# Kernel tuning notes

Hardware: AMD Instinct MI355X
Metric: run time of the kernel (lower is better)

The kernel has to match this reference:

```python
import jax, jax.numpy as jnp
import numpy as np

ALPHA = 0.2          # LeakyReLU negative slope
THRESHOLD = 0.5      # adjacency threshold
NEG_INF = -9e15      # same fill value as torch source


def setup_inputs() -> dict:
    key = jax.random.key(0)
    k_in, k_adj, k_W, k_a = jax.random.split(key, 4)
    B, N, C = 32, 1024, 64
    inp = jax.random.normal(k_in, (B, N, C), dtype=jnp.float32)
    adj = jax.random.uniform(k_adj, (N, N), dtype=jnp.float32)
    # xavier_uniform with gain=1.414 (as in torch init)
    gain = 1.414
    lim_W = gain * np.sqrt(6.0 / (C + C))
    W = jax.random.uniform(k_W, (C, C), dtype=jnp.float32, minval=-lim_W, maxval=lim_W)
    lim_a = gain * np.sqrt(6.0 / (2 * C + 1))
    a = jax.random.uniform(k_a, (2 * C, 1), dtype=jnp.float32, minval=-lim_a, maxval=lim_a)
    return {"input": inp, "adj": adj, "W": W, "a": a}


def reference(input, adj, W, a):
    # h: [B, N, C]
    h = jnp.matmul(input, W)
    C = W.shape[0]
    a_src = a[:C, 0]   # applied to h_i (row / query node)
    a_dst = a[C:, 0]   # applied to h_j (col / neighbor node)
    # Algebraic decomposition of a^T [h_i || h_j]: outer-sum of two [B,N] vectors.
    s_src = jnp.matmul(h, a_src)  # [B, N]
    s_dst = jnp.matmul(h, a_dst)  # [B, N]
    e = jax.nn.leaky_relu(s_src[:, :, None] + s_dst[:, None, :], negative_slope=ALPHA)  # [B,N,N]
    mask = adj > THRESHOLD  # [N, N], broadcast over batch
    attention = jax.nn.softmax(jnp.where(mask[None, :, :], e, NEG_INF), axis=2)
    h_prime = jnp.matmul(attention, h)  # [B, N, C]
    return jax.nn.elu(h_prime)
```

## Files before the change

kernel.cpp:

```cpp
#include <hip/hip_runtime.h>
#include <math.h>

#define ALPHA 0.2f
#define LOG2E 1.4426950408889634f

constexpr int B = 32, N = 1024, C = 64;

typedef __attribute__((ext_vector_type(8))) short short8;
typedef __attribute__((ext_vector_type(4))) float floatx4;

static __device__ __forceinline__ unsigned f32bf(float f) {
    unsigned u = __float_as_uint(f);
    return (u + 0x7FFFu + ((u >> 16) & 1u)) >> 16;
}

static __device__ __forceinline__ void async_copy16(void* lds_base, const void* g) {
    __builtin_amdgcn_global_load_lds(
        (const __attribute__((address_space(1))) unsigned int*)g,
        (__attribute__((address_space(3))) unsigned int*)lds_base, 16, 0, 0);
}

__global__ __launch_bounds__(256) void gat_pre(
    const float* __restrict__ input, const float* __restrict__ adj,
    const float* __restrict__ Wm, const float* __restrict__ a,
    unsigned short* __restrict__ hT, float* __restrict__ ssrc,
    float* __restrict__ sdst, unsigned long long* __restrict__ mask64)
{
    const int tid = threadIdx.x, lane = tid & 63, wave = tid >> 6;

    if (blockIdx.x >= 1024) {
        const int mb = blockIdx.x - 1024;
#pragma unroll
        for (int t = 0; t < 4; ++t) {
            const int id = mb * 16 + wave * 4 + t;
            const int i = id >> 4, jc = id & 15;
            const float av = adj[(size_t)i * N + jc * 64 + lane];
            const unsigned long long bal = __ballot(av > 0.5f);
            if (lane == 0) mask64[i * 16 + jc] = bal;
        }
        return;
    }

    __shared__ __align__(16) float W_l[64 * 65];
    __shared__ __align__(16) float a_l[128];
    __shared__ float wa_l[128];

    const int row0 = blockIdx.x * 32;
    const int b = row0 >> 10;
    const int jloc0 = row0 & 1023;
    const int m = lane & 15, kq = lane >> 4;

#pragma unroll
    for (int t = 0; t < 4; ++t) {
        const int t4 = tid + t * 256;
        const int base = t4 * 4;
        *(float4*)&W_l[(base >> 6) * 65 + (base & 63)] = ((const float4*)Wm)[t4];
    }
    if (tid < 32) ((float4*)a_l)[tid] = ((const float4*)a)[tid];

    float af[2][2][8];
#pragma unroll
    for (int at = 0; at < 2; ++at)
#pragma unroll
        for (int kc = 0; kc < 2; ++kc) {
            const float* src = &input[(size_t)(row0 + at * 16 + m) * 64 + kc * 32 + kq * 8];
            const float4 v0 = *(const float4*)src;
            const float4 v1 = *(const float4*)(src + 4);
            af[at][kc][0] = v0.x; af[at][kc][1] = v0.y; af[at][kc][2] = v0.z; af[at][kc][3] = v0.w;
            af[at][kc][4] = v1.x; af[at][kc][5] = v1.y; af[at][kc][6] = v1.z; af[at][kc][7] = v1.w;
        }

    __syncthreads();

    if (wave < 2) {
        const float* arow = a_l + wave * 64;
        float acc = 0.f;
        for (int t = 0; t < 64; ++t) {
            const int c = (t + lane) & 63;
            acc = fmaf(W_l[lane * 65 + c], arow[c], acc);
        }
        wa_l[wave * 64 + lane] = acc;
    }

    short8 bfr[2];
#pragma unroll
    for (int kc = 0; kc < 2; ++kc)
#pragma unroll
        for (int e = 0; e < 8; ++e)
            bfr[kc][e] = (short)f32bf(W_l[(kc * 32 + kq * 8 + e) * 65 + wave * 16 + m]);

    floatx4 acc[2] = {{0.f,0.f,0.f,0.f},{0.f,0.f,0.f,0.f}};
#pragma unroll
    for (int at = 0; at < 2; ++at) {
        short8 afr0, afr1;
#pragma unroll
        for (int e = 0; e < 8; ++e) {
            afr0[e] = (short)f32bf(af[at][0][e]);
            afr1[e] = (short)f32bf(af[at][1][e]);
        }
        acc[at] = __builtin_amdgcn_mfma_f32_16x16x32_bf16(afr0, bfr[0], acc[at], 0, 0, 0);
        acc[at] = __builtin_amdgcn_mfma_f32_16x16x32_bf16(afr1, bfr[1], acc[at], 0, 0, 0);
    }

    __syncthreads();

#pragma unroll
    for (int at = 0; at < 2; ++at) {
        float vs = 0.f, vd = 0.f;
#pragma unroll
        for (int kc = 0; kc < 2; ++kc)
#pragma unroll
            for (int e = 0; e < 8; ++e) {
                const float x = af[at][kc][e];
                vs = fmaf(x, wa_l[kc * 32 + kq * 8 + e], vs);
                vd = fmaf(x, wa_l[64 + kc * 32 + kq * 8 + e], vd);
            }
        vs += __shfl_xor(vs, 16, 64); vs += __shfl_xor(vs, 32, 64);
        vd += __shfl_xor(vd, 16, 64); vd += __shfl_xor(vd, 32, 64);
        if (wave == 0 && kq == 0) ssrc[row0 + at * 16 + m] = vs * LOG2E;
        if (wave == 1 && kq == 0) sdst[row0 + at * 16 + m] = vd * LOG2E;
    }

#pragma unroll
    for (int at = 0; at < 2; ++at) {
        const uint2 v = {f32bf(acc[at][0]) | (f32bf(acc[at][1]) << 16),
                         f32bf(acc[at][2]) | (f32bf(acc[at][3]) << 16)};
        const size_t off = ((size_t)(b * 64 + wave * 16 + m)) * 1024 + jloc0 + at * 16 + kq * 4;
        *(uint2*)&hT[off] = v;
    }
}

__global__ __launch_bounds__(256) void gat_attn(
    const unsigned short* __restrict__ hTg, const float* __restrict__ ssrc,
    const float* __restrict__ sdst, const unsigned char* __restrict__ maskB,
    float* __restrict__ out)
{
    __shared__ __align__(16) unsigned short h_u[64 * 64];
    __shared__ __align__(16) unsigned short p_u[32 * 64];
    __shared__ __align__(16) float sd_l[1024];
    __shared__ float psum_s[32];

    const int tid = threadIdx.x, lane = tid & 63, wave = tid >> 6;
    const int b = blockIdx.x & 31;
    const int i0 = (blockIdx.x >> 5) * 32;

    ((float4*)sd_l)[tid] = ((const float4*)(sdst + b * N))[tid];

    const int ii = tid >> 3, jo = tid & 7;
    const float ssq = ssrc[b * N + i0 + ii];
    const unsigned char* __restrict__ mrow = maskB + (size_t)(i0 + ii) * 128;

    unsigned mreg[4];
#pragma unroll
    for (int q = 0; q < 4; ++q) {
        unsigned v = 0;
#pragma unroll
        for (int t = 0; t < 4; ++t)
            v |= (unsigned)mrow[(q * 4 + t) * 8 + jo] << (t * 8);
        mreg[q] = v;
    }

    const int n16 = lane & 15, kq = lane >> 4;
    const int cB = wave * 16 + n16;
    const unsigned short* __restrict__ hTb = hTg + (size_t)b * 64 * 1024;

    const int rr = lane >> 3;
    const int sg = (lane & 7) ^ rr;
    const int pwoff = ii * 64 + (jo ^ (ii & 7)) * 8;

    floatx4 acc0 = {0.f,0.f,0.f,0.f}, acc1 = {0.f,0.f,0.f,0.f};
    float psacc = 0.f;

#pragma unroll
    for (int jt = 0; jt < 16; ++jt) {
        __syncthreads();

#pragma unroll
        for (int s = 0; s < 2; ++s) {
            const int r8 = wave * 16 + s * 8;
            async_copy16(&h_u[r8 * 64],
                         hTb + (size_t)(r8 + rr) * 1024 + jt * 64 + sg * 8);
        }

        const unsigned mb = (mreg[jt >> 2] >> ((jt & 3) * 8)) & 0xffu;
        const float4 s0 = *(const float4*)&sd_l[jt * 64 + jo * 8];
        const float4 s1 = *(const float4*)&sd_l[jt * 64 + jo * 8 + 4];
        const float ev[8] = {s0.x, s0.y, s0.z, s0.w, s1.x, s1.y, s1.z, s1.w};
        short8 pk;
        float loc = 0.f;
#pragma unroll
        for (int k = 0; k < 8; ++k) {
            float t = ssq + ev[k];
            t = t > 0.f ? t : ALPHA * t;
            const float p = ((mb >> k) & 1u) ? exp2f(t) : 0.f;
            loc += p;
            pk[k] = (short)f32bf(p);
        }
        psacc += loc;
        *(short8*)&p_u[pwoff] = pk;

        __syncthreads();

#pragma unroll
        for (int kc = 0; kc < 2; ++kc) {
            const int ch = ((kc * 4 + kq) ^ (cB & 7)) * 8;
            const int ca = ((kc * 4 + kq) ^ (n16 & 7)) * 8;
            const short8 bfr = *(const short8*)&h_u[cB * 64 + ch];
            const short8 a0  = *(const short8*)&p_u[n16 * 64 + ca];
            const short8 a1  = *(const short8*)&p_u[(16 + n16) * 64 + ca];
            acc0 = __builtin_amdgcn_mfma_f32_16x16x32_bf16(a0, bfr, acc0, 0, 0, 0);
            acc1 = __builtin_amdgcn_mfma_f32_16x16x32_bf16(a1, bfr, acc1, 0, 0, 0);
        }
    }

    psacc += __shfl_xor(psacc, 1, 64);
    psacc += __shfl_xor(psacc, 2, 64);
    psacc += __shfl_xor(psacc, 4, 64);
    if (jo == 0) psum_s[ii] = psacc;
    __syncthreads();

#pragma unroll
    for (int it = 0; it < 2; ++it) {
        const floatx4 acc = it ? acc1 : acc0;
#pragma unroll
        for (int r = 0; r < 4; ++r) {
            const int row = it * 16 + kq * 4 + r;
            const float hp = acc[r] / psum_s[row];
            const float o = hp > 0.f ? hp : __expf(hp) - 1.f;
            out[((size_t)(b * N + i0 + row)) * 64 + cB] = o;
        }
    }
}

extern "C" void kernel_launch(void* const* d_in, const int* in_sizes, int n_in,
                              void* d_out, int out_size, void* d_ws, size_t ws_size,
                              hipStream_t stream) {
    const float* input = (const float*)d_in[0];
    const float* adj   = (const float*)d_in[1];
    const float* Wm    = (const float*)d_in[2];
    const float* a     = (const float*)d_in[3];
    float* out = (float*)d_out;

    char* ws = (char*)d_ws;
    unsigned short* hT = (unsigned short*)ws;
    float* ssrc = (float*)(ws + 4194304);
    float* sdst = (float*)(ws + 4194304 + 131072);
    unsigned long long* mask64 = (unsigned long long*)(ws + 4194304 + 2 * 131072);

    gat_pre<<<2048, 256, 0, stream>>>(input, adj, Wm, a, hT, ssrc, sdst, mask64);
    gat_attn<<<1024, 256, 0, stream>>>(hT, ssrc, sdst, (const unsigned char*)mask64, out);
}
```

Measured before the change: 104.0 us.

## Fuse input projection into attention kernel with double-buffered LDS tiles

The pre-kernel now only converts input to bf16 and computes the source/destination scores via a folded W·a vector. The attention kernel recomputes h = input·W per 64-row tile with MFMA and writes it to LDS. It also uses double-buffered h/p tiles with a single barrier per iteration and prefetches the next input tile into registers. This removes the transposed h store and async LDS copy, but adds redundant projection work in every attention block and higher register pressure. Rounding is changed to a simpler round-half-up bf16 conversion.

```diff
diff --git a/kernel.cpp b/kernel.cpp
--- a/kernel.cpp
+++ b/kernel.cpp
@@ -9,27 +9,24 @@
 typedef __attribute__((ext_vector_type(8))) short short8;
 typedef __attribute__((ext_vector_type(4))) float floatx4;
 
-static __device__ __forceinline__ unsigned f32bf(float f) {
-    unsigned u = __float_as_uint(f);
-    return (u + 0x7FFFu + ((u >> 16) & 1u)) >> 16;
-}
-
-static __device__ __forceinline__ void async_copy16(void* lds_base, const void* g) {
-    __builtin_amdgcn_global_load_lds(
-        (const __attribute__((address_space(1))) unsigned int*)g,
-        (__attribute__((address_space(3))) unsigned int*)lds_base, 16, 0, 0);
+static __device__ __forceinline__ unsigned bfu(float f) {
+    return (__float_as_uint(f) + 0x8000u) >> 16;
+}
+static __device__ __forceinline__ unsigned pk2(float lo, float hi) {
+    return ((__float_as_uint(hi) + 0x8000u) & 0xFFFF0000u) |
+           ((__float_as_uint(lo) + 0x8000u) >> 16);
 }
 
 __global__ __launch_bounds__(256) void gat_pre(
     const float* __restrict__ input, const float* __restrict__ adj,
     const float* __restrict__ Wm, const float* __restrict__ a,
-    unsigned short* __restrict__ hT, float* __restrict__ ssrc,
+    unsigned short* __restrict__ inbf, float* __restrict__ ssrc,
     float* __restrict__ sdst, unsigned long long* __restrict__ mask64)
 {
     const int tid = threadIdx.x, lane = tid & 63, wave = tid >> 6;
 
-    if (blockIdx.x >= 1024) {
-        const int mb = blockIdx.x - 1024;
+    if (blockIdx.x < 1024) {
+        const int mb = blockIdx.x;
 #pragma unroll
         for (int t = 0; t < 4; ++t) {
             const int id = mb * 16 + wave * 4 + t;
@@ -41,102 +38,61 @@
         return;
     }
 
-    __shared__ __align__(16) float W_l[64 * 65];
-    __shared__ __align__(16) float a_l[128];
     __shared__ float wa_l[128];
-
-    const int row0 = blockIdx.x * 32;
-    const int b = row0 >> 10;
-    const int jloc0 = row0 & 1023;
-    const int m = lane & 15, kq = lane >> 4;
-
-#pragma unroll
-    for (int t = 0; t < 4; ++t) {
-        const int t4 = tid + t * 256;
-        const int base = t4 * 4;
-        *(float4*)&W_l[(base >> 6) * 65 + (base & 63)] = ((const float4*)Wm)[t4];
-    }
-    if (tid < 32) ((float4*)a_l)[tid] = ((const float4*)a)[tid];
-
-    float af[2][2][8];
-#pragma unroll
-    for (int at = 0; at < 2; ++at)
-#pragma unroll
-        for (int kc = 0; kc < 2; ++kc) {
-            const float* src = &input[(size_t)(row0 + at * 16 + m) * 64 + kc * 32 + kq * 8];
-            const float4 v0 = *(const float4*)src;
-            const float4 v1 = *(const float4*)(src + 4);
-            af[at][kc][0] = v0.x; af[at][kc][1] = v0.y; af[at][kc][2] = v0.z; af[at][kc][3] = v0.w;
-            af[at][kc][4] = v1.x; af[at][kc][5] = v1.y; af[at][kc][6] = v1.z; af[at][kc][7] = v1.w;
-        }
-
+    const int r0 = (blockIdx.x - 1024) * 32;
+
+    if (tid < 128) {
+        const int k = tid & 63, half = tid >> 6;
+        const float* __restrict__ ar = a + half * 64;
+        const float* __restrict__ wr = Wm + k * 64;
+        float acc = 0.f;
+#pragma unroll
+        for (int c4 = 0; c4 < 16; ++c4) {
+            const float4 wv = *(const float4*)&wr[c4 * 4];
+            const float4 av = *(const float4*)&ar[c4 * 4];
+            acc = fmaf(wv.x, av.x, fmaf(wv.y, av.y, fmaf(wv.z, av.z, fmaf(wv.w, av.w, acc))));
+        }
+        wa_l[half * 64 + k] = acc;
+    }
+
+    {
+        const float* __restrict__ src = input + (size_t)r0 * 64 + tid * 8;
+        const float4 v0 = *(const float4*)src;
+        const float4 v1 = *(const float4*)(src + 4);
+        uint4 o;
+        o.x = pk2(v0.x, v0.y); o.y = pk2(v0.z, v0.w);
+        o.z = pk2(v1.x, v1.y); o.w = pk2(v1.z, v1.w);
+        *(uint4*)&inbf[(size_t)r0 * 64 + tid * 8] = o;
+    }
     __syncthreads();
 
-    if (wave < 2) {
-        const float* arow = a_l + wave * 64;
-        float acc = 0.f;
-        for (int t = 0; t < 64; ++t) {
-            const int c = (t + lane) & 63;
-            acc = fmaf(W_l[lane * 65 + c], arow[c], acc);
-        }
-        wa_l[wave * 64 + lane] = acc;
-    }
-
-    short8 bfr[2];
-#pragma unroll
-    for (int kc = 0; kc < 2; ++kc)
-#pragma unroll
-        for (int e = 0; e < 8; ++e)
-            bfr[kc][e] = (short)f32bf(W_l[(kc * 32 + kq * 8 + e) * 65 + wave * 16 + m]);
-
-    floatx4 acc[2] = {{0.f,0.f,0.f,0.f},{0.f,0.f,0.f,0.f}};
-#pragma unroll
-    for (int at = 0; at < 2; ++at) {
-        short8 afr0, afr1;
-#pragma unroll
-        for (int e = 0; e < 8; ++e) {
-            afr0[e] = (short)f32bf(af[at][0][e]);
-            afr1[e] = (short)f32bf(af[at][1][e]);
-        }
-        acc[at] = __builtin_amdgcn_mfma_f32_16x16x32_bf16(afr0, bfr[0], acc[at], 0, 0, 0);
-        acc[at] = __builtin_amdgcn_mfma_f32_16x16x32_bf16(afr1, bfr[1], acc[at], 0, 0, 0);
-    }
-
-    __syncthreads();
-
-#pragma unroll
-    for (int at = 0; at < 2; ++at) {
+    {
+        const int row = r0 + (tid >> 3), seg = tid & 7;
+        const float4 x0 = *(const float4*)&input[(size_t)row * 64 + seg * 8];
+        const float4 x1 = *(const float4*)&input[(size_t)row * 64 + seg * 8 + 4];
         float vs = 0.f, vd = 0.f;
-#pragma unroll
-        for (int kc = 0; kc < 2; ++kc)
-#pragma unroll
-            for (int e = 0; e < 8; ++e) {
-                const float x = af[at][kc][e];
-                vs = fmaf(x, wa_l[kc * 32 + kq * 8 + e], vs);
-                vd = fmaf(x, wa_l[64 + kc * 32 + kq * 8 + e], vd);
-            }
-        vs += __shfl_xor(vs, 16, 64); vs += __shfl_xor(vs, 32, 64);
-        vd += __shfl_xor(vd, 16, 64); vd += __shfl_xor(vd, 32, 64);
-        if (wave == 0 && kq == 0) ssrc[row0 + at * 16 + m] = vs * LOG2E;
-        if (wave == 1 && kq == 0) sdst[row0 + at * 16 + m] = vd * LOG2E;
-    }
-
-#pragma unroll
-    for (int at = 0; at < 2; ++at) {
-        const uint2 v = {f32bf(acc[at][0]) | (f32bf(acc[at][1]) << 16),
-                         f32bf(acc[at][2]) | (f32bf(acc[at][3]) << 16)};
-        const size_t off = ((size_t)(b * 64 + wave * 16 + m)) * 1024 + jloc0 + at * 16 + kq * 4;
-        *(uint2*)&hT[off] = v;
+        const float4 w0 = *(const float4*)&wa_l[seg * 8];
+        const float4 w1 = *(const float4*)&wa_l[seg * 8 + 4];
+        const float4 d0 = *(const float4*)&wa_l[64 + seg * 8];
+        const float4 d1 = *(const float4*)&wa_l[64 + seg * 8 + 4];
+        vs = fmaf(x0.x, w0.x, fmaf(x0.y, w0.y, fmaf(x0.z, w0.z, fmaf(x0.w, w0.w, vs))));
+        vs = fmaf(x1.x, w1.x, fmaf(x1.y, w1.y, fmaf(x1.z, w1.z, fmaf(x1.w, w1.w, vs))));
+        vd = fmaf(x0.x, d0.x, fmaf(x0.y, d0.y, fmaf(x0.z, d0.z, fmaf(x0.w, d0.w, vd))));
+        vd = fmaf(x1.x, d1.x, fmaf(x1.y, d1.y, fmaf(x1.z, d1.z, fmaf(x1.w, d1.w, vd))));
+        vs += __shfl_xor(vs, 1, 64); vd += __shfl_xor(vd, 1, 64);
+        vs += __shfl_xor(vs, 2, 64); vd += __shfl_xor(vd, 2, 64);
+        vs += __shfl_xor(vs, 4, 64); vd += __shfl_xor(vd, 4, 64);
+        if (seg == 0) { ssrc[row] = vs * LOG2E; sdst[row] = vd * LOG2E; }
     }
 }
 
 __global__ __launch_bounds__(256) void gat_attn(
-    const unsigned short* __restrict__ hTg, const float* __restrict__ ssrc,
-    const float* __restrict__ sdst, const unsigned char* __restrict__ maskB,
-    float* __restrict__ out)
+    const unsigned short* __restrict__ inbf, const float* __restrict__ Wm,
+    const float* __restrict__ ssrc, const float* __restrict__ sdst,
+    const unsigned char* __restrict__ maskB, float* __restrict__ out)
 {
-    __shared__ __align__(16) unsigned short h_u[64 * 64];
-    __shared__ __align__(16) unsigned short p_u[32 * 64];
+    __shared__ __align__(16) unsigned short h_u[2][64 * 64];
+    __shared__ __align__(16) unsigned short p_u[2][32 * 64];
     __shared__ __align__(16) float sd_l[1024];
     __shared__ float psum_s[32];
 
@@ -149,7 +105,6 @@
     const int ii = tid >> 3, jo = tid & 7;
     const float ssq = ssrc[b * N + i0 + ii];
     const unsigned char* __restrict__ mrow = maskB + (size_t)(i0 + ii) * 128;
-
     unsigned mreg[4];
 #pragma unroll
     for (int q = 0; q < 4; ++q) {
@@ -162,52 +117,79 @@
 
     const int n16 = lane & 15, kq = lane >> 4;
     const int cB = wave * 16 + n16;
-    const unsigned short* __restrict__ hTb = hTg + (size_t)b * 64 * 1024;
-
-    const int rr = lane >> 3;
-    const int sg = (lane & 7) ^ rr;
+    const unsigned short* __restrict__ Ab = inbf + (size_t)b * 1024 * 64;
+
+    short8 wf[2];
+#pragma unroll
+    for (int kc = 0; kc < 2; ++kc)
+#pragma unroll
+        for (int e = 0; e < 8; ++e)
+            wf[kc][e] = (short)bfu(Wm[(kc * 32 + kq * 8 + e) * 64 + cB]);
+
     const int pwoff = ii * 64 + (jo ^ (ii & 7)) * 8;
+    int hwo[4];
+#pragma unroll
+    for (int ms = 0; ms < 4; ++ms)
+        hwo[ms] = cB * 64 + (((ms * 2 + (kq >> 1)) ^ (cB & 7)) * 8) + (kq & 1) * 4;
+
+    auto loadA = [&](int jt, short8 af[4][2]) {
+#pragma unroll
+        for (int ms = 0; ms < 4; ++ms)
+#pragma unroll
+            for (int kc = 0; kc < 2; ++kc)
+                af[ms][kc] = *(const short8*)&Ab[(size_t)(jt * 64 + ms * 16 + n16) * 64 + kc * 32 + kq * 8];
+    };
 
     floatx4 acc0 = {0.f,0.f,0.f,0.f}, acc1 = {0.f,0.f,0.f,0.f};
     float psacc = 0.f;
-
-#pragma unroll
+    short8 afn[4][2];
+    loadA(0, afn);
+    __syncthreads();
+
+#pragma unroll 2
     for (int jt = 0; jt < 16; ++jt) {
+        const int buf = jt & 1;
+        short8 afc[4][2];
+#pragma unroll
+        for (int ms = 0; ms < 4; ++ms) { afc[ms][0] = afn[ms][0]; afc[ms][1] = afn[ms][1]; }
+        if (jt < 15) loadA(jt + 1, afn);
+
+#pragma unroll
+        for (int ms = 0; ms < 4; ++ms) {
+            floatx4 ha = {0.f,0.f,0.f,0.f};
+            ha = __builtin_amdgcn_mfma_f32_16x16x32_bf16(afc[ms][0], wf[0], ha, 0, 0, 0);
+            ha = __builtin_amdgcn_mfma_f32_16x16x32_bf16(afc[ms][1], wf[1], ha, 0, 0, 0);
+            const uint2 hv = {pk2(ha[0], ha[1]), pk2(ha[2], ha[3])};
+            *(uint2*)&h_u[buf][hwo[ms]] = hv;
+        }
+
+        {
+            const unsigned mb = (mreg[jt >> 2] >> ((jt & 3) * 8)) & 0xffu;
+            const float4 s0 = *(const float4*)&sd_l[jt * 64 + jo * 8];
+            const float4 s1 = *(const float4*)&sd_l[jt * 64 + jo * 8 + 4];
+            const float ev[8] = {s0.x, s0.y, s0.z, s0.w, s1.x, s1.y, s1.z, s1.w};
+            float p[8];
+            float loc = 0.f;
+#pragma unroll
+            for (int k = 0; k < 8; ++k) {
+                float t = ssq + ev[k];
+                t = fmaxf(t, ALPHA * t);
+                p[k] = ((mb >> k) & 1u) ? exp2f(t) : 0.f;
+                loc += p[k];
+            }
+            psacc += loc;
+            const uint4 pw = {pk2(p[0], p[1]), pk2(p[2], p[3]), pk2(p[4], p[5]), pk2(p[6], p[7])};
+            *(uint4*)&p_u[buf][pwoff] = pw;
+        }
+
         __syncthreads();
 
 #pragma unroll
-        for (int s = 0; s < 2; ++s) {
-            const int r8 = wave * 16 + s * 8;
-            async_copy16(&h_u[r8 * 64],
-                         hTb + (size_t)(r8 + rr) * 1024 + jt * 64 + sg * 8);
-        }
-
-        const unsigned mb = (mreg[jt >> 2] >> ((jt & 3) * 8)) & 0xffu;
-        const float4 s0 = *(const float4*)&sd_l[jt * 64 + jo * 8];
-        const float4 s1 = *(const float4*)&sd_l[jt * 64 + jo * 8 + 4];
-        const float ev[8] = {s0.x, s0.y, s0.z, s0.w, s1.x, s1.y, s1.z, s1.w};
-        short8 pk;
-        float loc = 0.f;
-#pragma unroll
-        for (int k = 0; k < 8; ++k) {
-            float t = ssq + ev[k];
-            t = t > 0.f ? t : ALPHA * t;
-            const float p = ((mb >> k) & 1u) ? exp2f(t) : 0.f;
-            loc += p;
-            pk[k] = (short)f32bf(p);
-        }
-        psacc += loc;
-        *(short8*)&p_u[pwoff] = pk;
-
-        __syncthreads();
-
-#pragma unroll
         for (int kc = 0; kc < 2; ++kc) {
-            const int ch = ((kc * 4 + kq) ^ (cB & 7)) * 8;
-            const int ca = ((kc * 4 + kq) ^ (n16 & 7)) * 8;
-            const short8 bfr = *(const short8*)&h_u[cB * 64 + ch];
-            const short8 a0  = *(const short8*)&p_u[n16 * 64 + ca];
-            const short8 a1  = *(const short8*)&p_u[(16 + n16) * 64 + ca];
+            const int ch = (kc * 4 + kq);
+            const short8 bfr = *(const short8*)&h_u[buf][cB * 64 + ((ch ^ (cB & 7)) * 8)];
+            const short8 a0  = *(const short8*)&p_u[buf][n16 * 64 + ((ch ^ (n16 & 7)) * 8)];
+            const short8 a1  = *(const short8*)&p_u[buf][(16 + n16) * 64 + ((ch ^ (n16 & 7)) * 8)];
             acc0 = __builtin_amdgcn_mfma_f32_16x16x32_bf16(a0, bfr, acc0, 0, 0, 0);
             acc1 = __builtin_amdgcn_mfma_f32_16x16x32_bf16(a1, bfr, acc1, 0, 0, 0);
         }
@@ -242,11 +224,11 @@
     float* out = (float*)d_out;
 
     char* ws = (char*)d_ws;
-    unsigned short* hT = (unsigned short*)ws;
+    unsigned short* inbf = (unsigned short*)ws;
     float* ssrc = (float*)(ws + 4194304);
     float* sdst = (float*)(ws + 4194304 + 131072);
     unsigned long long* mask64 = (unsigned long long*)(ws + 4194304 + 2 * 131072);
 
-    gat_pre<<<2048, 256, 0, stream>>>(input, adj, Wm, a, hT, ssrc, sdst, mask64);
-    gat_attn<<<1024, 256, 0, stream>>>(hT, ssrc, sdst, (const unsigned char*)mask64, out);
-}
+    gat_pre<<<2048, 256, 0, stream>>>(input, adj, Wm, a, inbf, ssrc, sdst, mask64);
+    gat_attn<<<1024, 256, 0, stream>>>(inbf, Wm, ssrc, sdst, (const unsigned char*)mask64, out);
+}
```

Result: slower. 132.8 us (+27.8%).
